# Performance work log

Hardware: AMD Instinct MI355X
Metric: run time of the kernel (lower is better)

Reference implementation:

```python
import jax, jax.numpy as jnp
from jax import lax
import numpy as np

DT = jnp.float32
M = 1000          # quadrature points (torch.linspace steps=1000)
PI = float(np.pi)
EPS = 1e-12       # guards sqrt args against round-off (original asserts instead)


def _trapz(f, x):
    dx = x[1:] - x[:-1]
    return jnp.sum(0.5 * (f[..., 1:] + f[..., :-1]) * dx, axis=-1)


def _ygrid():
    return jnp.linspace(0.001, 0.999, M, dtype=DT)


def _extend(y, integ):
    # prepend linearly-extrapolated value at y=0, append 0 at y=1 (as in torch code)
    slope = (integ[..., 1] - integ[..., 0]) / (y[1] - y[0])
    v0 = integ[..., 0] - slope * y[0]
    yy = jnp.concatenate([jnp.zeros((1,), DT), y, jnp.ones((1,), DT)])
    zrs = jnp.zeros(integ.shape[:-1] + (1,), DT)
    ii = jnp.concatenate([v0[..., None], integ, zrs], axis=-1)
    return yy, ii


def eval_f(a, z):
    _a = jnp.concatenate([jnp.ones((1,), DT), a])  # [1, a0, a1]
    out = jnp.zeros_like(z)
    for i in range(3):
        for j in range(3):
            c = _a[i] * _a[j]
            if i + j == 4:
                out = out - 4.0 * c * z**4 * jnp.log(z)
            else:
                out = out + 4.0 * c * (z**4 - z**(i + j)) / (i + j - 4)
    return out


def eval_df(a, z):
    _a = jnp.concatenate([jnp.ones((1,), DT), a])
    out = jnp.zeros_like(z)
    for i in range(3):
        for j in range(3):
            out = out - 4.0 * _a[i] * _a[j] * z**(i + j)
    return (out + 4.0 * eval_f(a, z)) / z


def _bcoef(a, b):
    last = a.sum() - b.sum()
    return jnp.concatenate([jnp.ones((1,), DT), b, last[None]])  # length 4


def eval_b_(a, b, z):
    c = _bcoef(a, b)
    out = jnp.zeros_like(z)
    for i in range(4):
        for j in range(4):
            out = out + c[i] * c[j] * z**(i + j)
    return out


def eval_db(a, b, z):
    c = _bcoef(a, b)
    x = jnp.zeros_like(z)
    dx = jnp.zeros_like(z)
    for i in range(4):
        x = x + c[i] * z**i
    for i in range(1, 4):
        dx = dx + i * c[i] * z**(i - 1)
    return 2.0 * dx * x


def eval_g(a, b, z):
    return eval_b_(a, b, z) / ((1 - z) * (1 + z) * (1 + z**2))


def eval_dg(a, b, z):
    D = (1 - z) * (1 + z) * (1 + z**2)  # = 1 - z^4
    return eval_db(a, b, z) / D + 4.0 * z**3 * eval_b_(a, b, z) / D**2


def integrate_L(a, b, zs):
    y = _ygrid()
    zs_ = zs[..., None]
    z = zs_ * (1 - y) * (1 + y)
    sqrtg = jnp.sqrt(eval_g(a, b, z))
    f_over_fs = eval_f(a, z) / eval_f(a, zs_)
    arg = f_over_fs / ((1 - y)**4 * (1 + y)**4) - 1.0
    integ = sqrtg / jnp.sqrt(jnp.maximum(arg, EPS)) * y
    yy, ii = _extend(y, integ)
    return 4.0 * zs * _trapz(ii, yy) / PI


def integrate_dL(a, b, zs):
    y = _ygrid()
    zs_ = zs[..., None]
    z = zs_ * (1 - y) * (1 + y)
    fs = eval_f(a, zs_)
    g = eval_g(a, b, z)
    f_over_fs = eval_f(a, z) / fs
    df = eval_df(a, z)
    dfs = eval_df(a, zs_)
    dg = eval_dg(a, b, z)
    r4 = zs_**4 / z**4
    integ = r4 * f_over_fs * (zs_ * dfs / fs + 2 + z * dg / g) - zs_**4 / z**3 * df / fs - 2 - z * dg / g
    integ = integ * 2 * jnp.sqrt(jnp.maximum(1 - z / zs_, 0.0)) * jnp.sqrt(g) / jnp.maximum(r4 * f_over_fs - 1, EPS)**1.5
    yy, ii = _extend(y, integ)
    return _trapz(ii, yy) / PI


def integrate_V(a, b, logcoef, zs):
    coef = jnp.exp(logcoef)
    # connected piece
    y = _ygrid()
    zs_ = zs[..., None]
    z = zs_ * (1 - y) * (1 + y)
    f = eval_f(a, z)
    fg = f * eval_g(a, b, z)
    f_over_fs = f / eval_f(a, zs_)
    w = (1 - y)**2 * (1 + y)**2
    integ = jnp.sqrt(jnp.maximum(fg, EPS)) / w * (1.0 / jnp.sqrt(jnp.maximum(1 - w**2 / f_over_fs, EPS)) - 1.0) * y
    yy, ii = _extend(y, integ)
    Vc = coef * PI * 4.0 * _trapz(ii, yy) / zs
    # disconnected piece
    y2 = jnp.linspace(0.001, 1.0, M, dtype=DT)
    z2 = 1 - (1 - zs_) * y2
    fg2 = eval_f(a, z2) * eval_g(a, b, z2)
    integ2 = jnp.sqrt(jnp.maximum(fg2, EPS)) / z2**2
    yy2 = jnp.concatenate([jnp.zeros((1,), DT), y2])
    ii2 = jnp.concatenate([jnp.ones(integ2.shape[:-1] + (1,), DT), integ2], axis=-1)
    Vd = coef * PI * 2.0 * (1 - zs) * _trapz(ii2, yy2)
    return Vc - Vd


def _bisect(fun, lo, hi, iters=30):
    # keeps invariant fun(lo) >= 0 > fun(hi); matches the torch bisections
    def body(_, c):
        lo, hi = c
        mid = 0.5 * (lo + hi)
        pred = fun(mid) < 0
        return (jnp.where(pred, lo, mid), jnp.where(pred, mid, hi))
    lo, hi = lax.fori_loop(0, iters, body, (jnp.asarray(lo, DT), jnp.asarray(hi, DT)))
    return 0.5 * (lo + hi)


def get_L_max(a, b):
    zs = _bisect(lambda m: integrate_dL(a, b, m), 0.001, 0.999)
    return zs, integrate_L(a, b, zs)


def get_L_crit(a, b, logcoef, zs_max):
    zs = _bisect(lambda m: -integrate_V(a, b, logcoef, m), 0.001, zs_max)
    return zs, integrate_L(a, b, zs)


def find_zs_newton(a, b, L, init, steps=25):
    @jax.checkpoint
    def step(zs, _):
        Lz = integrate_L(a, b, zs)
        dL = integrate_dL(a, b, zs)
        zs = jnp.clip(zs - (Lz - L) / dL, 1e-4, 0.9995)
        return zs, None
    zs, _ = lax.scan(step, init, None, length=steps)
    return zs


def forward(Ls, a, b, logcoef):
    # bisection searches run under torch.no_grad in the original -> stop gradients
    a_ng = lax.stop_gradient(a)
    b_ng = lax.stop_gradient(b)
    lc_ng = lax.stop_gradient(logcoef)
    zs_max, L_max = get_L_max(a_ng, b_ng)
    zs_crit, L_crit = get_L_crit(a_ng, b_ng, lc_ng, zs_max)
    valid = Ls < L_crit
    L_eff = jnp.where(valid, Ls, 0.5 * L_crit)  # masked rows still solve a well-posed problem
    init = jnp.clip(L_eff / L_max * zs_max, 1e-4, 0.9995)  # interp1d through (0,0)-(L_max, zs_max)
    zs = find_zs_newton(a, b, L_eff, init)
    V = integrate_V(a, b, logcoef, zs)
    return jnp.where(valid, V, jnp.zeros_like(V))


def setup_inputs() -> dict:
    key = jax.random.key(0)
    k1, k2, k3 = jax.random.split(key, 3)
    B = 4096
    Ls = jax.random.uniform(k1, (B,), dtype=jnp.float32) * 0.2
    a = 0.05 * jax.random.normal(k2, (2,), dtype=jnp.float32)
    b = 0.05 * jax.random.normal(k3, (2,), dtype=jnp.float32)
    logcoef = jnp.zeros((), jnp.float32)
    return {"Ls": Ls, "a": a, "b": b, "logcoef": logcoef}


def reference(Ls, a, b, logcoef):
    return forward(Ls, a, b, logcoef)
```

## Files before the change

kernel.cpp:

```cpp
#include <hip/hip_runtime.h>
#include <math.h>

#define MQ 1000
#define PI_F 3.14159265358979323846f
#define EPSF 1e-12f
#define DYF  ((float)(0.998/999.0))
#define DY2F ((float)(0.999/999.0))
#define NG   2048
#define HG   (0.998f / (float)NG)
#define ZT   0.006f

__device__ __forceinline__ float frcp(float x)  { return __builtin_amdgcn_rcpf(x); }
__device__ __forceinline__ float frsq(float x)  { return __builtin_amdgcn_rsqf(x); }
__device__ __forceinline__ float fsqrt(float x) { return __builtin_amdgcn_sqrtf(x); }


struct Co {
    float q1, q2, q3, q4, cf4;
    float e1, e2, e3, e4;
    float b0, b1, p3;
    float coef;
};

__device__ __forceinline__ Co make_co(const float* a, const float* b, const float* lc) {
    Co c;
    float a0 = a[0], a1 = a[1];
    float cf1 = -8.f * a0 / 3.f;
    float cf2 = -2.f * (2.f * a1 + a0 * a0);
    float cf3 = -8.f * a0 * a1;
    c.cf4 = -4.f * a1 * a1;
    c.q1 = -cf1; c.q2 = -cf2; c.q3 = -cf3; c.q4 = cf1 + cf2 + cf3 - 1.f;
    c.e1 = 2.f * a0;
    c.e2 = 2.f * a1 + a0 * a0;
    c.e3 = 2.f * a0 * a1;
    c.e4 = a1 * a1;
    c.b0 = b[0]; c.b1 = b[1];
    c.p3 = a0 + a1 - b[0] - b[1];
    c.coef = expf(lc[0]);
    return c;
}

struct Uni { float zs, fs, rfs, A4; };

__device__ __forceinline__ Uni make_uni(const Co& c, float zs) {
    Uni U; U.zs = zs;
    float z = zs;
    float lg = __logf(z);
    float t4 = c.q4 + c.cf4 * lg;
    float fz = 1.f + z * (c.q1 + z * (c.q2 + z * (c.q3 + z * t4)));
    float s  = 1.f + z * (c.e1 + z * (c.e2 + z * (c.e3 + z * c.e4)));
    U.fs = fz;
    U.rfs = frcp(fz);
    float dfs = 4.f * (fz - s) * frcp(z);
    U.A4 = zs * dfs * U.rfs - 2.f;
    return U;
}

__device__ __forceinline__ void point_LdL(const Co& c, const Uni& U,
                                          float y, float u,
                                          float& iL, float& iD) {
    float u2  = u * u;
    float ru2 = frcp(u2);
    float ru4 = ru2 * ru2;
    float z  = U.zs * u;
    float z2 = z * z, z4 = z2 * z2;
    float lg = __logf(z);
    float t4 = c.q4 + c.cf4 * lg;
    float fz = 1.f + z * (c.q1 + z * (c.q2 + z * (c.q3 + z * t4)));
    float s  = 1.f + z * (c.e1 + z * (c.e2 + z * (c.e3 + z * c.e4)));
    float P  = 1.f + z * (c.b0 + z * (c.b1 + z * c.p3));
    float dP = c.b0 + z * (2.f * c.b1 + z * (3.f * c.p3));
    float D  = 1.f - z4;
    float rsqD = frsq(D);
    float rcpD = rsqD * rsqD;
    float rcpP = frcp(P);
    float zdgg = 2.f * z * dP * rcpP + 4.f * z4 * rcpD;
    float F4 = fz * U.rfs * ru4;
    float S4 = s  * U.rfs * ru4;
    float den = fmaxf(F4 - 1.f, EPSF);
    float rs  = frsq(den);
    float sqg = P * rsqD;
    float t1  = sqg * rs;
    iL = t1 * y;
    float t = F4 * (U.A4 + zdgg) + 4.f * S4 - 2.f - zdgg;
    float rs2 = rs * rs;
    iD = t * (2.f * y) * (t1 * rs2);
}

__device__ __forceinline__ float point_Vc(const Co& c, const Uni& U,
                                          float y, float u) {
    float u2  = u * u;
    float u4  = u2 * u2;
    float ru2 = frcp(u2);
    float z  = U.zs * u;
    float z2 = z * z, z4 = z2 * z2;
    float lg = __logf(z);
    float t4 = c.q4 + c.cf4 * lg;
    float fz = 1.f + z * (c.q1 + z * (c.q2 + z * (c.q3 + z * t4)));
    float P  = 1.f + z * (c.b0 + z * (c.b1 + z * c.p3));
    float D  = 1.f - z4;
    float rsqD = frsq(D);
    float rcpD = rsqD * rsqD;
    float fg = fz * P * P * rcpD;
    float sqfg = fsqrt(fmaxf(fg, EPSF));
    float rfz = frcp(fz);
    float arg = fmaxf(1.f - u4 * U.fs * rfz, EPSF);
    float t = frsq(arg) - 1.f;
    return sqfg * ru2 * t * y;
}

__device__ __forceinline__ float point_Vd(const Co& c, const Uni& U, float y2) {
    float z  = 1.f - (1.f - U.zs) * y2;
    float z2 = z * z, z4 = z2 * z2;
    float lg = __logf(z);
    float t4 = c.q4 + c.cf4 * lg;
    float fz = 1.f + z * (c.q1 + z * (c.q2 + z * (c.q3 + z * t4)));
    float P  = 1.f + z * (c.b0 + z * (c.b1 + z * c.p3));
    float D  = 1.f - z4;
    float rsqD = frsq(D);
    float fg = fz * P * P * (rsqD * rsqD);
    float sq = fsqrt(fmaxf(fg, EPSF));
    float rz = frcp(z);
    return sq * rz * rz;
}

__device__ __forceinline__ float trapz_ext(float S, float i0, float i1, float iN) {
    float slope = (i1 - i0) * frcp(DYF);
    float v0 = i0 - slope * 0.001f;
    float yLast = 0.001f + 999.f * DYF;
    return DYF * (S - 0.5f * (i0 + iN))
         + 0.5f * (v0 + i0) * 0.001f
         + 0.5f * iN * (1.f - yLast);
}

__device__ __forceinline__ float trapz_d(float S, float q0, float qN) {
    return 0.5f * (1.f + q0) * 0.001f + DY2F * (S - 0.5f * (q0 + qN));
}

__global__ __launch_bounds__(128) void grid_eval_kernel(
        const float* a, const float* b, const float* lc, float* ws) {
    __shared__ float red[4];
    __shared__ float spx[8];
    int bid = blockIdx.x;
    int t = threadIdx.x, lane = t & 63, w = t >> 6;
    Co c = make_co(a, b, lc);
    int i = (bid < NG) ? bid : bid - NG;
    float zq = fmaf((float)i + 0.5f, HG, 0.001f);
    Uni U = make_uni(c, zq);

    if (bid < NG) {
        float sL = 0.f, sD = 0.f, l0 = 0.f, d0 = 0.f, l1 = 0.f, d1 = 0.f,
              lN = 0.f, dN = 0.f;
#pragma unroll
        for (int k = 0; k < 8; ++k) {
            if (k < 7 || t < 104) {
                int j = t + 128 * k;
                float y = fmaf((float)j, DYF, 0.001f);
                float u = 1.f - y * y;
                float iL, iD;
                point_LdL(c, U, y, u, iL, iD);
                sL += iL; sD += iD;
                if (k == 0) {
                    if (t == 0) { l0 = iL; d0 = iD; }
                    if (t == 1) { l1 = iL; d1 = iD; }
                }
                if (k == 7 && t == 103) { lN = iL; dN = iD; }
            }
        }
#pragma unroll
        for (int o = 32; o > 0; o >>= 1) {
            sL += __shfl_xor(sL, o, 64);
            sD += __shfl_xor(sD, o, 64);
        }
        if (lane == 0) { red[w] = sL; red[2 + w] = sD; }
        if (t == 0)   { spx[0] = l0; spx[3] = d0; }
        if (t == 1)   { spx[1] = l1; spx[4] = d1; }
        if (t == 103) { spx[2] = lN; spx[5] = dN; }
        __syncthreads();
        if (t == 0) {
            float SL = red[0] + red[1], SD = red[2] + red[3];
            float Lv  = 4.f * zq * trapz_ext(SL, spx[0], spx[1], spx[2]) / PI_F;
            float dLv = trapz_ext(SD, spx[3], spx[4], spx[5]) / PI_F;
            ws[16 + i] = dLv;
            ws[16 + 2 * NG + i] = Lv;
        }
    } else {
        float sc = 0.f, sd = 0.f, c0 = 0.f, c1v = 0.f, cN = 0.f,
              q0 = 0.f, qN = 0.f;
#pragma unroll
        for (int k = 0; k < 8; ++k) {
            if (k < 7 || t < 104) {
                int j = t + 128 * k;
                float y = fmaf((float)j, DYF, 0.001f);
                float u = 1.f - y * y;
                float vc = point_Vc(c, U, y, u);
                float y2 = fmaf((float)j, DY2F, 0.001f);
                float vd = point_Vd(c, U, y2);
                sc += vc; sd += vd;
                if (k == 0) {
                    if (t == 0) { c0 = vc; q0 = vd; }
                    if (t == 1) { c1v = vc; }
                }
                if (k == 7 && t == 103) { cN = vc; qN = vd; }
            }
        }
#pragma unroll
        for (int o = 32; o > 0; o >>= 1) {
            sc += __shfl_xor(sc, o, 64);
            sd += __shfl_xor(sd, o, 64);
        }
        if (lane == 0) { red[w] = sc; red[2 + w] = sd; }
        if (t == 0)   { spx[0] = c0; spx[3] = q0; }
        if (t == 1)   { spx[1] = c1v; }
        if (t == 103) { spx[2] = cN; spx[4] = qN; }
        __syncthreads();
        if (t == 0) {
            float Sc = red[0] + red[1], Sd = red[2] + red[3];
            float Vc = c.coef * PI_F * 4.f * trapz_ext(Sc, spx[0], spx[1], spx[2]) * frcp(zq);
            float Vd = c.coef * PI_F * 2.f * (1.f - zq) * trapz_d(Sd, spx[3], spx[4]);
            ws[16 + NG + i] = Vc - Vd;
        }
    }
}

__global__ __launch_bounds__(256) void scan_kernel(float* ws) {
    __shared__ int sdl, sv;
    const float* dLbuf = ws + 16;
    const float* Vbuf  = ws + 16 + NG;
    const float* Lbuf  = ws + 16 + 2 * NG;
    int t = threadIdx.x;
    if (t == 0) { sdl = NG; sv = NG; }
    __syncthreads();
#pragma unroll
    for (int r = 0; r < NG / 256; ++r) {
        int i = t + 256 * r;
        float dcur = dLbuf[i];
        float dprev = (i > 0) ? dLbuf[i - 1] : 1.f;
        if (dcur < 0.f && dprev >= 0.f) atomicMin(&sdl, i);
        float vcur = Vbuf[i];
        float vprev = (i > 0) ? Vbuf[i - 1] : -1.f;
        if (vcur > 0.f && vprev <= 0.f) atomicMin(&sv, i);
    }
    __syncthreads();
    if (t == 0) {
        int bound = sdl, iv = sv;
        float Lcrit;
        if (bound < 2) {
            Lcrit = -1.f;
        } else if (iv >= NG || iv >= bound) {
            Lcrit = Lbuf[bound - 1];
        } else if (iv == 0) {
            float z0 = 0.001f + 0.5f * HG;
            Lcrit = Lbuf[0] * 0.001f * frcp(z0);
        } else {
            float zhi = fmaf((float)iv + 0.5f, HG, 0.001f);
            float zlo = zhi - HG;
            float vhi = Vbuf[iv], vlo = Vbuf[iv - 1];
            float zc = zlo - vlo * (zhi - zlo) * frcp(fmaxf(vhi - vlo, 1e-30f));
            zc = fminf(fmaxf(zc, zlo), zhi);
            float tt = (zc - 0.001f) * frcp(HG) - 0.5f;
            int i0 = (int)tt;
            i0 = max(0, min(i0, bound - 2));
            float frac = fminf(fmaxf(tt - (float)i0, 0.f), 1.f);
            Lcrit = Lbuf[i0] + frac * (Lbuf[i0 + 1] - Lbuf[i0]);
        }
        ws[0] = Lcrit;
        ws[1] = (float)bound;
    }
}

__global__ __launch_bounds__(128) void elem_v_kernel(
        const float* Ls, const float* a, const float* b, const float* lc,
        const float* ws, float* out, int B) {
    __shared__ float red[4];
    __shared__ float spx[8];
    int wid = blockIdx.x;
    int t = threadIdx.x, lane = t & 63, w = t >> 6;
    if (wid >= B) return;

    float L_crit = ws[0];
    int bound = (int)ws[1];
    float Lq = Ls[wid];
    if (!(Lq < L_crit) || bound < 2) {
        if (t == 0) out[wid] = 0.f;
        return;
    }

    const float* dLbuf = ws + 16;
    const float* Vbuf  = ws + 16 + NG;
    const float* Lbuf  = ws + 16 + 2 * NG;
    int lo = -1, hi = bound - 1;
    while (hi > lo) {
        int mid = (lo + hi + 1) >> 1;
        if (Lbuf[mid] < Lq) lo = mid; else hi = mid - 1;
    }
    float zs;
    if (lo < 0) {
        float z0 = 0.001f + 0.5f * HG;
        zs = z0 * Lq * frcp(fmaxf(Lbuf[0], 1e-20f));
    } else {
        int seg = min(lo, bound - 2);
        float zl = fmaf((float)seg + 0.5f, HG, 0.001f);
        float Ll = Lbuf[seg],  Lh = Lbuf[seg + 1];
        float dl = dLbuf[seg] * HG, dh = dLbuf[seg + 1] * HG;
        float s = fminf(fmaxf((Lq - Ll) * frcp(fmaxf(Lh - Ll, 1e-20f)), 0.f), 1.f);
#pragma unroll
        for (int it = 0; it < 2; ++it) {
            float s2 = s * s, s3 = s2 * s;
            float H  = (2.f*s3 - 3.f*s2 + 1.f) * Ll + (s3 - 2.f*s2 + s) * dl
                     + (-2.f*s3 + 3.f*s2) * Lh + (s3 - s2) * dh;
            float Hp = (6.f*s2 - 6.f*s) * (Ll - Lh)
                     + (3.f*s2 - 4.f*s + 1.f) * dl + (3.f*s2 - 2.f*s) * dh;
            float step = (H - Lq) * frcp(Hp);
            if (fabsf(Hp) > 1e-20f) s = fminf(fmaxf(s - step, 0.f), 1.f);
        }
        zs = fmaf(s, HG, zl);
    }
    zs = fminf(fmaxf(zs, 1e-4f), 0.9995f);

    if (zs >= ZT) {
        if (t == 0) {
            float tt = (zs - 0.001f) * frcp(HG) - 0.5f;
            int i0 = (int)tt;
            i0 = max(1, min(i0, NG - 3));
            float s = tt - (float)i0;
            float vm = Vbuf[i0 - 1], v0 = Vbuf[i0], v1 = Vbuf[i0 + 1], v2 = Vbuf[i0 + 2];
            float wm = -s * (s - 1.f) * (s - 2.f) * (1.f / 6.f);
            float w0 = (s + 1.f) * (s - 1.f) * (s - 2.f) * 0.5f;
            float w1 = -(s + 1.f) * s * (s - 2.f) * 0.5f;
            float w2 = (s + 1.f) * s * (s - 1.f) * (1.f / 6.f);
            out[wid] = wm * vm + w0 * v0 + w1 * v1 + w2 * v2;
        }
        return;
    }

    Co c = make_co(a, b, lc);
    Uni U = make_uni(c, zs);
    float sc = 0.f, sd = 0.f, c0 = 0.f, c1v = 0.f, cN = 0.f, q0 = 0.f, qN = 0.f;
#pragma unroll
    for (int k = 0; k < 8; ++k) {
        if (k < 7 || t < 104) {
            int j = t + 128 * k;
            float y = fmaf((float)j, DYF, 0.001f);
            float u = 1.f - y * y;
            float vc = point_Vc(c, U, y, u);
            float y2 = fmaf((float)j, DY2F, 0.001f);
            float vd = point_Vd(c, U, y2);
            sc += vc; sd += vd;
            if (k == 0) {
                if (t == 0) { c0 = vc; q0 = vd; }
                if (t == 1) { c1v = vc; }
            }
            if (k == 7 && t == 103) { cN = vc; qN = vd; }
        }
    }
#pragma unroll
    for (int o = 32; o > 0; o >>= 1) {
        sc += __shfl_xor(sc, o, 64);
        sd += __shfl_xor(sd, o, 64);
    }
    if (lane == 0) { red[w] = sc; red[2 + w] = sd; }
    if (t == 0)   { spx[0] = c0; spx[3] = q0; }
    if (t == 1)   { spx[1] = c1v; }
    if (t == 103) { spx[2] = cN; spx[4] = qN; }
    __syncthreads();
    if (t == 0) {
        float Sc = red[0] + red[1], Sd = red[2] + red[3];
        float Vc = c.coef * PI_F * 4.f * trapz_ext(Sc, spx[0], spx[1], spx[2]) * frcp(zs);
        float Vd = c.coef * PI_F * 2.f * (1.f - zs) * trapz_d(Sd, spx[3], spx[4]);
        out[wid] = Vc - Vd;
    }
}

extern "C" void kernel_launch(void* const* d_in, const int* in_sizes, int n_in,
                              void* d_out, int out_size, void* d_ws, size_t ws_size,
                              hipStream_t stream) {
    const float* Ls = (const float*)d_in[0];
    const float* a  = (const float*)d_in[1];
    const float* b  = (const float*)d_in[2];
    const float* lc = (const float*)d_in[3];
    float* out = (float*)d_out;
    float* ws  = (float*)d_ws;
    int B = in_sizes[0];

    grid_eval_kernel<<<2 * NG, 128, 0, stream>>>(a, b, lc, ws);
    scan_kernel<<<1, 256, 0, stream>>>(ws);
    elem_v_kernel<<<B, 128, 0, stream>>>(Ls, a, b, lc, ws, out, B);
}
```

Before: 84.67 us.

## Fuse L/dL and V grid integrals into one block and halve grid resolution

Blocks that evaluated L/dL and blocks that evaluated V at the same z grid point are merged into one block. The shared intermediates (z, log, polynomial f, P, D) are now computed once per quadrature point. The coarse z grid used for the scan and initial guesses is also halved from 2048 to 1024 points, so the first kernel does roughly a quarter of the original work. The coarser grid can change the bracketing and initial guesses that later kernels use, and the fused block carries more live registers.

```diff
diff --git a/kernel.cpp b/kernel.cpp
--- a/kernel.cpp
+++ b/kernel.cpp
@@ -6,7 +6,7 @@
 #define EPSF 1e-12f
 #define DYF  ((float)(0.998/999.0))
 #define DY2F ((float)(0.999/999.0))
-#define NG   2048
+#define NG   1024
 #define HG   (0.998f / (float)NG)
 #define ZT   0.006f
 
@@ -56,10 +56,11 @@
     return U;
 }
 
-__device__ __forceinline__ void point_LdL(const Co& c, const Uni& U,
+__device__ __forceinline__ void point_all(const Co& c, const Uni& U,
                                           float y, float u,
-                                          float& iL, float& iD) {
+                                          float& iL, float& iD, float& vc) {
     float u2  = u * u;
+    float u4  = u2 * u2;
     float ru2 = frcp(u2);
     float ru4 = ru2 * ru2;
     float z  = U.zs * u;
@@ -82,9 +83,15 @@
     float sqg = P * rsqD;
     float t1  = sqg * rs;
     iL = t1 * y;
-    float t = F4 * (U.A4 + zdgg) + 4.f * S4 - 2.f - zdgg;
+    float tnum = F4 * (U.A4 + zdgg) + 4.f * S4 - 2.f - zdgg;
     float rs2 = rs * rs;
-    iD = t * (2.f * y) * (t1 * rs2);
+    iD = tnum * (2.f * y) * (t1 * rs2);
+    float fg = fz * P * P * rcpD;
+    float sqfg = fsqrt(fmaxf(fg, EPSF));
+    float rfz = frcp(fz);
+    float arg = fmaxf(1.f - u4 * U.fs * rfz, EPSF);
+    float tv = frsq(arg) - 1.f;
+    vc = sqfg * ru2 * tv * y;
 }
 
 __device__ __forceinline__ float point_Vc(const Co& c, const Uni& U,
@@ -139,87 +146,57 @@
 
 __global__ __launch_bounds__(128) void grid_eval_kernel(
         const float* a, const float* b, const float* lc, float* ws) {
-    __shared__ float red[4];
-    __shared__ float spx[8];
-    int bid = blockIdx.x;
+    __shared__ float red[8];
+    __shared__ float spx[12];
+    int i = blockIdx.x;
     int t = threadIdx.x, lane = t & 63, w = t >> 6;
     Co c = make_co(a, b, lc);
-    int i = (bid < NG) ? bid : bid - NG;
     float zq = fmaf((float)i + 0.5f, HG, 0.001f);
     Uni U = make_uni(c, zq);
 
-    if (bid < NG) {
-        float sL = 0.f, sD = 0.f, l0 = 0.f, d0 = 0.f, l1 = 0.f, d1 = 0.f,
-              lN = 0.f, dN = 0.f;
-#pragma unroll
-        for (int k = 0; k < 8; ++k) {
-            if (k < 7 || t < 104) {
-                int j = t + 128 * k;
-                float y = fmaf((float)j, DYF, 0.001f);
-                float u = 1.f - y * y;
-                float iL, iD;
-                point_LdL(c, U, y, u, iL, iD);
-                sL += iL; sD += iD;
-                if (k == 0) {
-                    if (t == 0) { l0 = iL; d0 = iD; }
-                    if (t == 1) { l1 = iL; d1 = iD; }
-                }
-                if (k == 7 && t == 103) { lN = iL; dN = iD; }
+    float sL = 0.f, sD = 0.f, sc = 0.f, sd = 0.f;
+    float l0 = 0.f, l1 = 0.f, lN = 0.f, d0 = 0.f, d1 = 0.f, dN = 0.f;
+    float c0 = 0.f, c1v = 0.f, cN = 0.f, q0 = 0.f, qN = 0.f;
+#pragma unroll
+    for (int k = 0; k < 8; ++k) {
+        if (k < 7 || t < 104) {
+            int j = t + 128 * k;
+            float y = fmaf((float)j, DYF, 0.001f);
+            float u = 1.f - y * y;
+            float iL, iD, vc;
+            point_all(c, U, y, u, iL, iD, vc);
+            float y2 = fmaf((float)j, DY2F, 0.001f);
+            float vd = point_Vd(c, U, y2);
+            sL += iL; sD += iD; sc += vc; sd += vd;
+            if (k == 0) {
+                if (t == 0) { l0 = iL; d0 = iD; c0 = vc; q0 = vd; }
+                if (t == 1) { l1 = iL; d1 = iD; c1v = vc; }
             }
-        }
-#pragma unroll
-        for (int o = 32; o > 0; o >>= 1) {
-            sL += __shfl_xor(sL, o, 64);
-            sD += __shfl_xor(sD, o, 64);
-        }
-        if (lane == 0) { red[w] = sL; red[2 + w] = sD; }
-        if (t == 0)   { spx[0] = l0; spx[3] = d0; }
-        if (t == 1)   { spx[1] = l1; spx[4] = d1; }
-        if (t == 103) { spx[2] = lN; spx[5] = dN; }
-        __syncthreads();
-        if (t == 0) {
-            float SL = red[0] + red[1], SD = red[2] + red[3];
-            float Lv  = 4.f * zq * trapz_ext(SL, spx[0], spx[1], spx[2]) / PI_F;
-            float dLv = trapz_ext(SD, spx[3], spx[4], spx[5]) / PI_F;
-            ws[16 + i] = dLv;
-            ws[16 + 2 * NG + i] = Lv;
-        }
-    } else {
-        float sc = 0.f, sd = 0.f, c0 = 0.f, c1v = 0.f, cN = 0.f,
-              q0 = 0.f, qN = 0.f;
-#pragma unroll
-        for (int k = 0; k < 8; ++k) {
-            if (k < 7 || t < 104) {
-                int j = t + 128 * k;
-                float y = fmaf((float)j, DYF, 0.001f);
-                float u = 1.f - y * y;
-                float vc = point_Vc(c, U, y, u);
-                float y2 = fmaf((float)j, DY2F, 0.001f);
-                float vd = point_Vd(c, U, y2);
-                sc += vc; sd += vd;
-                if (k == 0) {
-                    if (t == 0) { c0 = vc; q0 = vd; }
-                    if (t == 1) { c1v = vc; }
-                }
-                if (k == 7 && t == 103) { cN = vc; qN = vd; }
-            }
-        }
-#pragma unroll
-        for (int o = 32; o > 0; o >>= 1) {
-            sc += __shfl_xor(sc, o, 64);
-            sd += __shfl_xor(sd, o, 64);
-        }
-        if (lane == 0) { red[w] = sc; red[2 + w] = sd; }
-        if (t == 0)   { spx[0] = c0; spx[3] = q0; }
-        if (t == 1)   { spx[1] = c1v; }
-        if (t == 103) { spx[2] = cN; spx[4] = qN; }
-        __syncthreads();
-        if (t == 0) {
-            float Sc = red[0] + red[1], Sd = red[2] + red[3];
-            float Vc = c.coef * PI_F * 4.f * trapz_ext(Sc, spx[0], spx[1], spx[2]) * frcp(zq);
-            float Vd = c.coef * PI_F * 2.f * (1.f - zq) * trapz_d(Sd, spx[3], spx[4]);
-            ws[16 + NG + i] = Vc - Vd;
-        }
+            if (k == 7 && t == 103) { lN = iL; dN = iD; cN = vc; qN = vd; }
+        }
+    }
+#pragma unroll
+    for (int o = 32; o > 0; o >>= 1) {
+        sL += __shfl_xor(sL, o, 64);
+        sD += __shfl_xor(sD, o, 64);
+        sc += __shfl_xor(sc, o, 64);
+        sd += __shfl_xor(sd, o, 64);
+    }
+    if (lane == 0) { red[w] = sL; red[2 + w] = sD; red[4 + w] = sc; red[6 + w] = sd; }
+    if (t == 0)   { spx[0] = l0; spx[3] = d0; spx[6] = c0; spx[9]  = q0; }
+    if (t == 1)   { spx[1] = l1; spx[4] = d1; spx[7] = c1v; }
+    if (t == 103) { spx[2] = lN; spx[5] = dN; spx[8] = cN; spx[10] = qN; }
+    __syncthreads();
+    if (t == 0) {
+        float SL = red[0] + red[1], SD = red[2] + red[3];
+        float Sc = red[4] + red[5], Sd = red[6] + red[7];
+        float Lv  = 4.f * zq * trapz_ext(SL, spx[0], spx[1], spx[2]) / PI_F;
+        float dLv = trapz_ext(SD, spx[3], spx[4], spx[5]) / PI_F;
+        float Vcn = c.coef * PI_F * 4.f * trapz_ext(Sc, spx[6], spx[7], spx[8]) * frcp(zq);
+        float Vd  = c.coef * PI_F * 2.f * (1.f - zq) * trapz_d(Sd, spx[9], spx[10]);
+        ws[16 + i] = dLv;
+        ws[16 + NG + i] = Vcn - Vd;
+        ws[16 + 2 * NG + i] = Lv;
     }
 }
 
@@ -383,7 +360,7 @@
     float* ws  = (float*)d_ws;
     int B = in_sizes[0];
 
-    grid_eval_kernel<<<2 * NG, 128, 0, stream>>>(a, b, lc, ws);
+    grid_eval_kernel<<<NG, 128, 0, stream>>>(a, b, lc, ws);
     scan_kernel<<<1, 256, 0, stream>>>(ws);
     elem_v_kernel<<<B, 128, 0, stream>>>(Ls, a, b, lc, ws, out, B);
 }
```

After: 78.35 us. -7.5%, faster.
